# Performance work log

Hardware: AMD Instinct MI355X
Metric: run time of the kernel (lower is better)

Reference implementation:

```python
import jax, jax.numpy as jnp
import numpy as np
import math

POOL = 7          # RoIAlign output_size
SR = 2            # sampling_ratio


def _roi_align(feat, boxes, bidx):
    """torchvision RoIAlign, aligned=False, spatial_scale=1.0, sampling_ratio=2.
    feat: [B,C,H,W]; boxes: [N,4] (x1,y1,x2,y2) in pixel coords of this level;
    bidx: [N] int batch indices. Returns [N,C,POOL,POOL]."""
    B, C, H, W = feat.shape
    x1, y1, x2, y2 = boxes[:, 0], boxes[:, 1], boxes[:, 2], boxes[:, 3]
    roi_w = jnp.maximum(x2 - x1, 1.0)
    roi_h = jnp.maximum(y2 - y1, 1.0)
    bin_w = roi_w / POOL
    bin_h = roi_h / POOL
    # sample-point offsets within the ROI, in bin units: [POOL, SR]
    off = jnp.arange(POOL, dtype=feat.dtype)[:, None] + (jnp.arange(SR, dtype=feat.dtype)[None, :] + 0.5) / SR
    ys = y1[:, None, None] + bin_h[:, None, None] * off  # [N,POOL,SR]
    xs = x1[:, None, None] + bin_w[:, None, None] * off  # [N,POOL,SR]

    def prep(c, size):
        valid = (c > -1.0) & (c < size)
        c = jnp.clip(c, 0.0, size - 1)
        lo = jnp.floor(c).astype(jnp.int32)
        hi = jnp.minimum(lo + 1, size - 1)
        return lo, hi, c - lo, valid

    y_lo, y_hi, fy, vy = prep(ys, H)
    x_lo, x_hi, fx, vx = prep(xs, W)

    b = bidx.astype(jnp.int32)[:, None, None, None, None]  # [N,1,1,1,1]

    def gather(yi, xi):
        # -> [N,POOL,SR,POOL,SR,C] (advanced indices broadcast, channel slice last)
        return feat[b, :, yi[:, :, :, None, None], xi[:, None, None, :, :]]

    hy = (1.0 - fy)[:, :, :, None, None, None]
    ly = fy[:, :, :, None, None, None]
    hx = (1.0 - fx)[:, None, None, :, :, None]
    lx = fx[:, None, None, :, :, None]
    v = (gather(y_lo, x_lo) * hy * hx + gather(y_lo, x_hi) * hy * lx
         + gather(y_hi, x_lo) * ly * hx + gather(y_hi, x_hi) * ly * lx)
    valid = (vy[:, :, :, None, None] & vx[:, None, None, :, :])[..., None]
    v = jnp.where(valid, v, 0.0)
    out = v.mean(axis=(2, 4))          # average over SRxSR samples -> [N,POOL,POOL,C]
    return out.transpose(0, 3, 1, 2)   # [N,C,POOL,POOL]


def setup_inputs() -> dict:
    key = jax.random.key(0)
    k2, k3, k4, k5, kxy, kwh, kbi = jax.random.split(key, 7)
    N = 1000
    p2 = jax.random.normal(k2, (2, 256, 256, 256), dtype=jnp.float32)
    p3 = jax.random.normal(k3, (2, 256, 128, 128), dtype=jnp.float32)
    p4 = jax.random.normal(k4, (2, 256, 64, 64), dtype=jnp.float32)
    p5 = jax.random.normal(k5, (2, 256, 32, 32), dtype=jnp.float32)
    xy = jax.random.uniform(kxy, (N, 2), minval=0.0, maxval=0.7)
    wh = jax.random.uniform(kwh, (N, 2), minval=0.02, maxval=0.3)
    rpn_bbox = jnp.concatenate([xy, xy + wh], axis=1)  # (x1,y1,x2,y2) normalized
    box_index = jax.random.randint(kbi, (N,), 0, 2, dtype=jnp.int32)
    return {"p2": p2, "p3": p3, "p4": p4, "p5": p5,
            "rpn_bbox": rpn_bbox, "box_index": box_index}


def reference(p2, p3, p4, p5, rpn_bbox, box_index):
    feats = [p2, p3, p4, p5]
    N = rpn_bbox.shape[0]
    x1, y1, x2, y2 = rpn_bbox[:, 0], rpn_bbox[:, 1], rpn_bbox[:, 2], rpn_bbox[:, 3]
    area = (y2 - y1) * (x2 - x1)
    roi_level = jnp.log(jnp.sqrt(area)) / math.log(2.0)
    roi_level = jnp.clip(jnp.round(roi_level) + 4.0, 0.0, 3.0).astype(jnp.int32)
    # Compute RoIAlign of every ROI at every level, then select per-ROI level.
    # (The masked-select / per-level dispatch / argsort-combine in the original
    # restores original ROI order, so this is mathematically identical.)
    pooled_per_level = jnp.stack(
        [_roi_align(f, rpn_bbox * f.shape[3], box_index) for f in feats], axis=0
    )  # [4, N, C, 7, 7]
    pooled = pooled_per_level[roi_level, jnp.arange(N)]  # [N, C, 7, 7]
    return pooled
```

## Files before the change

### kernel.cpp

```cpp
#include <hip/hip_runtime.h>
#include <math.h>

#define POOL 7
#define NCELL 49
#define NCH 256
#define CH_SPLIT 8
#define CHPB (NCH / CH_SPLIT)
#define CHPW (CHPB / 4)
#define LDSF 640
#define NIT_S 10

typedef __attribute__((address_space(1))) void global_void;
typedef __attribute__((address_space(3))) void lds_void;
__device__ __forceinline__ void stage4(const float* g, float* l) {
    __builtin_amdgcn_global_load_lds((global_void*)g, (lds_void*)l, 4, 0, 0);
}
__device__ __forceinline__ void stage16(const float* g, float* l) {
    __builtin_amdgcn_global_load_lds((global_void*)g, (lds_void*)l, 16, 0, 0);
}

struct Tab {
    int loff0[4], loff1[4];
    float w00[4], w01[4], w10[4], w11[4];
};

__device__ __forceinline__ void make_tab(Tab& tb, int lane, int W, int rs, int xb, int y0,
                                         float x1, float y1, float bin_w, float bin_h)
{
    int cell = (lane < NCELL) ? lane : (NCELL - 1);
    int py = cell / POOL, px = cell % POOL;
#pragma unroll
    for (int s = 0; s < 4; ++s) {
        int sy = s >> 1, sx = s & 1;
        float y = y1 + bin_h * ((float)py + ((float)sy + 0.5f) * 0.5f);
        float x = x1 + bin_w * ((float)px + ((float)sx + 0.5f) * 0.5f);
        bool v = (y > -1.f) && (y < (float)W) && (x > -1.f) && (x < (float)W);
        float yc = fminf(fmaxf(y, 0.f), (float)(W - 1));
        float xc = fminf(fmaxf(x, 0.f), (float)(W - 1));
        int ylo = (int)floorf(yc), xlo = (int)floorf(xc);
        int yhi = min(ylo + 1, W - 1);
        float fy = yc - (float)ylo, fx = xc - (float)xlo;
        float vv = v ? 0.25f : 0.f;
        int bxp = min(xlo, W - 2);
        bool in = (xlo == bxp);
        float wx0 = in ? (1.f - fx) : 0.f;
        float wx1 = in ? fx : 1.f;
        float wr0 = (1.f - fy) * vv, wr1 = fy * vv;
        tb.loff0[s] = (ylo - y0) * rs + (bxp - xb);
        tb.loff1[s] = (yhi - y0) * rs + (bxp - xb);
        tb.w00[s] = wr0 * wx0; tb.w01[s] = wr0 * wx1;
        tb.w10[s] = wr1 * wx0; tb.w11[s] = wr1 * wx1;
    }
}

__device__ __forceinline__ float consume(const float* cb, const Tab& tb)
{
    float acc = 0.f;
#pragma unroll
    for (int s = 0; s < 4; ++s) {
        float a0 = cb[tb.loff0[s]], a1 = cb[tb.loff0[s] + 1];
        float b0 = cb[tb.loff1[s]], b1 = cb[tb.loff1[s] + 1];
        acc += tb.w00[s] * a0 + tb.w01[s] * a1 + tb.w10[s] * b0 + tb.w11[s] * b1;
    }
    return acc;
}

template <int NIT4>
__device__ __forceinline__ void box_x4(
    const float* fbase, float* outp, float* sm, int lane,
    int W, int HW, int wwa, int y0, int x0a, int ngrp,
    float x1, float y1, float bin_w, float bin_h)
{
    int g_off[NIT4];
    bool act[NIT4];
    int wwa4 = wwa >> 2;
#pragma unroll
    for (int k = 0; k < NIT4; ++k) {
        int idx = k * 64 + lane;
        act[k] = idx < ngrp;
        int ii = act[k] ? idx : 0;
        int r = ii / wwa4;
        int c = ii - r * wwa4;
        g_off[k] = (y0 + r) * W + x0a + c * 4;
    }
#pragma unroll
    for (int k = 0; k < NIT4; ++k)
        if (act[k]) stage16(fbase + g_off[k], sm + k * 256);

    Tab tb;
    make_tab(tb, lane, W, wwa, x0a, y0, x1, y1, bin_w, bin_h);

#pragma unroll 2
    for (int i = 0; i < CHPW; ++i) {
        if (i + 1 < CHPW) {
            const float* fc = fbase + (size_t)(i + 1) * HW;
            float* nb = sm + ((i + 1) & 1) * LDSF;
#pragma unroll
            for (int k = 0; k < NIT4; ++k)
                if (act[k]) stage16(fc + g_off[k], nb + k * 256);
            if constexpr (NIT4 == 1) asm volatile("s_waitcnt vmcnt(1)" ::: "memory");
            else if constexpr (NIT4 == 2) asm volatile("s_waitcnt vmcnt(2)" ::: "memory");
            else                          asm volatile("s_waitcnt vmcnt(3)" ::: "memory");
        } else {
            asm volatile("s_waitcnt vmcnt(0)" ::: "memory");
        }
        float acc = consume(sm + (i & 1) * LDSF, tb);
        if (lane < NCELL)
            __builtin_nontemporal_store(acc, outp + (size_t)i * NCELL);
    }
}

__device__ __forceinline__ void box_s(
    const float* fbase, float* outp, float* sm, int lane,
    int W, int HW, int ww, int y0, int x0, int packed,
    float x1, float y1, float bin_w, float bin_h)
{
    int g_off[NIT_S];
#pragma unroll
    for (int k = 0; k < NIT_S; ++k) {
        int idx = k * 64 + lane;
        idx = (idx < packed) ? idx : 0;
        int r = idx / ww;
        int c = idx - r * ww;
        g_off[k] = (y0 + r) * W + (x0 + c);
    }
#pragma unroll
    for (int k = 0; k < NIT_S; ++k) stage4(fbase + g_off[k], sm + k * 64);

    Tab tb;
    make_tab(tb, lane, W, ww, x0, y0, x1, y1, bin_w, bin_h);

#pragma unroll 2
    for (int i = 0; i < CHPW; ++i) {
        if (i + 1 < CHPW) {
            const float* fc = fbase + (size_t)(i + 1) * HW;
            float* nb = sm + ((i + 1) & 1) * LDSF;
#pragma unroll
            for (int k = 0; k < NIT_S; ++k) stage4(fc + g_off[k], nb + k * 64);
            asm volatile("s_waitcnt vmcnt(10)" ::: "memory");
        } else {
            asm volatile("s_waitcnt vmcnt(0)" ::: "memory");
        }
        float acc = consume(sm + (i & 1) * LDSF, tb);
        if (lane < NCELL)
            __builtin_nontemporal_store(acc, outp + (size_t)i * NCELL);
    }
}

__global__ __launch_bounds__(256, 8) void roi_align_fpn_kernel(
    const float* __restrict__ p2, const float* __restrict__ p3,
    const float* __restrict__ p4, const float* __restrict__ p5,
    const float* __restrict__ boxes, const int* __restrict__ bidx,
    float* __restrict__ out, int N)
{
    __shared__ float smem[4][2][LDSF];
    const int n = blockIdx.y;
    const int t = threadIdx.x;
    const int wave = t >> 6;
    const int lane = t & 63;

    float bx1 = boxes[4 * n + 0], by1 = boxes[4 * n + 1];
    float bx2 = boxes[4 * n + 2], by2 = boxes[4 * n + 3];
    float area = (by2 - by1) * (bx2 - bx1);
    float lvlf = logf(sqrtf(area)) * 1.4426950408889634f;
    int level = (int)fminf(fmaxf(rintf(lvlf) + 4.0f, 0.0f), 3.0f);
    int W = 256 >> level;
    int HW = W * W;
    float scale = (float)W;
    float x1 = bx1 * scale, y1 = by1 * scale;
    float bin_w = fmaxf((bx2 - bx1) * scale, 1.0f) * (1.0f / POOL);
    float bin_h = fmaxf((by2 - by1) * scale, 1.0f) * (1.0f / POOL);

    const float* feat = (level == 0) ? p2 : (level == 1) ? p3 : (level == 2) ? p4 : p5;
    feat += (size_t)bidx[n] * NCH * HW;

    float yA = y1 + bin_h * 0.25f, yB = y1 + bin_h * 6.75f;
    float xA = x1 + bin_w * 0.25f, xB = x1 + bin_w * 6.75f;
    int y0  = (int)floorf(fminf(fmaxf(yA, 0.f), (float)(W - 1)));
    int y1h = min((int)floorf(fminf(fmaxf(yB, 0.f), (float)(W - 1))) + 1, W - 1);
    int x0  = (int)floorf(fminf(fmaxf(xA, 0.f), (float)(W - 1)));
    x0 = min(x0, W - 2);
    int x1p = min((int)floorf(fminf(fmaxf(xB, 0.f), (float)(W - 1))) + 1, W - 1);
    int ww = x1p - x0 + 1;
    int wh = y1h - y0 + 1;

    int x0a = x0 & ~3;
    int wwa = ((x1p - x0a + 1) + 3) & ~3;
    if ((wwa & 15) == 0) wwa += 4;
    int padded = wwa * wh;

    const int ch0 = blockIdx.x * CHPB + wave * CHPW;
    const float* fbase = feat + (size_t)ch0 * HW;
    float* sm = &smem[wave][0][0];
    int cell = (lane < NCELL) ? lane : (NCELL - 1);
    float* outp = out + (size_t)n * NCH * NCELL + (size_t)ch0 * NCELL + cell;

    if (padded <= LDSF) {
        int ngrp = (wwa >> 2) * wh;
        int nit4 = (ngrp + 63) >> 6;
        if (nit4 == 1)      box_x4<1>(fbase, outp, sm, lane, W, HW, wwa, y0, x0a, ngrp, x1, y1, bin_w, bin_h);
        else if (nit4 == 2) box_x4<2>(fbase, outp, sm, lane, W, HW, wwa, y0, x0a, ngrp, x1, y1, bin_w, bin_h);
        else                box_x4<3>(fbase, outp, sm, lane, W, HW, wwa, y0, x0a, ngrp, x1, y1, bin_w, bin_h);
    } else {
        int whc = min(wh, LDSF / ww);
        int packed = ww * whc;
        box_s(fbase, outp, sm, lane, W, HW, ww, y0, x0, packed, x1, y1, bin_w, bin_h);
    }
}

extern "C" void kernel_launch(void* const* d_in, const int* in_sizes, int n_in,
                              void* d_out, int out_size, void* d_ws, size_t ws_size,
                              hipStream_t stream) {
    const float* p2    = (const float*)d_in[0];
    const float* p3    = (const float*)d_in[1];
    const float* p4    = (const float*)d_in[2];
    const float* p5    = (const float*)d_in[3];
    const float* boxes = (const float*)d_in[4];
    const int*   bidx  = (const int*)d_in[5];
    float* out = (float*)d_out;
    int N = in_sizes[5];
    dim3 grid(CH_SPLIT, N);
    roi_align_fpn_kernel<<<grid, 256, 0, stream>>>(p2, p3, p4, p5, boxes, bidx, out, N);
}
```

Measured before the change: 274.5 us.

## Sort ROIs by level, batch and spatial bucket for cache locality; peel first iteration

Adds a single-block counting-sort kernel that orders boxes by FPN level, batch index and a coarse 8x8 center grid, then indexes the main kernel through this permutation. Spatially nearby ROIs run close together in time so their overlapping feature windows are more likely to hit in L2/MALL. The first channel iteration of both staging loops is also peeled, and the vmcnt waits are changed to allow one more outstanding operation, leaving the previous iteration's store in flight. The cost is an extra serial one-block launch and an indirection load per block.

```diff
diff --git a/kernel.cpp b/kernel.cpp
--- a/kernel.cpp
+++ b/kernel.cpp
@@ -9,6 +9,7 @@
 #define CHPW (CHPB / 4)
 #define LDSF 640
 #define NIT_S 10
+#define NBUCK 512
 
 typedef __attribute__((address_space(1))) void global_void;
 typedef __attribute__((address_space(3))) void lds_void;
@@ -17,6 +18,16 @@
 }
 __device__ __forceinline__ void stage16(const float* g, float* l) {
     __builtin_amdgcn_global_load_lds((global_void*)g, (lds_void*)l, 16, 0, 0);
+}
+
+template <int V> __device__ __forceinline__ void vwait() {
+    if constexpr (V == 0)  asm volatile("s_waitcnt vmcnt(0)" ::: "memory");
+    else if constexpr (V == 1)  asm volatile("s_waitcnt vmcnt(1)" ::: "memory");
+    else if constexpr (V == 2)  asm volatile("s_waitcnt vmcnt(2)" ::: "memory");
+    else if constexpr (V == 3)  asm volatile("s_waitcnt vmcnt(3)" ::: "memory");
+    else if constexpr (V == 4)  asm volatile("s_waitcnt vmcnt(4)" ::: "memory");
+    else if constexpr (V == 10) asm volatile("s_waitcnt vmcnt(10)" ::: "memory");
+    else if constexpr (V == 11) asm volatile("s_waitcnt vmcnt(11)" ::: "memory");
 }
 
 struct Tab {
@@ -90,19 +101,27 @@
     Tab tb;
     make_tab(tb, lane, W, wwa, x0a, y0, x1, y1, bin_w, bin_h);
 
+    {
+        const float* fc = fbase + (size_t)HW;
+        float* nb = sm + LDSF;
+#pragma unroll
+        for (int k = 0; k < NIT4; ++k)
+            if (act[k]) stage16(fc + g_off[k], nb + k * 256);
+        vwait<NIT4>();
+        float acc = consume(sm, tb);
+        if (lane < NCELL) __builtin_nontemporal_store(acc, outp);
+    }
 #pragma unroll 2
-    for (int i = 0; i < CHPW; ++i) {
+    for (int i = 1; i < CHPW; ++i) {
         if (i + 1 < CHPW) {
             const float* fc = fbase + (size_t)(i + 1) * HW;
             float* nb = sm + ((i + 1) & 1) * LDSF;
 #pragma unroll
             for (int k = 0; k < NIT4; ++k)
                 if (act[k]) stage16(fc + g_off[k], nb + k * 256);
-            if constexpr (NIT4 == 1) asm volatile("s_waitcnt vmcnt(1)" ::: "memory");
-            else if constexpr (NIT4 == 2) asm volatile("s_waitcnt vmcnt(2)" ::: "memory");
-            else                          asm volatile("s_waitcnt vmcnt(3)" ::: "memory");
+            vwait<NIT4 + 1>();
         } else {
-            asm volatile("s_waitcnt vmcnt(0)" ::: "memory");
+            vwait<1>();
         }
         float acc = consume(sm + (i & 1) * LDSF, tb);
         if (lane < NCELL)
@@ -130,16 +149,25 @@
     Tab tb;
     make_tab(tb, lane, W, ww, x0, y0, x1, y1, bin_w, bin_h);
 
+    {
+        const float* fc = fbase + (size_t)HW;
+        float* nb = sm + LDSF;
+#pragma unroll
+        for (int k = 0; k < NIT_S; ++k) stage4(fc + g_off[k], nb + k * 64);
+        vwait<NIT_S>();
+        float acc = consume(sm, tb);
+        if (lane < NCELL) __builtin_nontemporal_store(acc, outp);
+    }
 #pragma unroll 2
-    for (int i = 0; i < CHPW; ++i) {
+    for (int i = 1; i < CHPW; ++i) {
         if (i + 1 < CHPW) {
             const float* fc = fbase + (size_t)(i + 1) * HW;
             float* nb = sm + ((i + 1) & 1) * LDSF;
 #pragma unroll
             for (int k = 0; k < NIT_S; ++k) stage4(fc + g_off[k], nb + k * 64);
-            asm volatile("s_waitcnt vmcnt(10)" ::: "memory");
+            vwait<NIT_S + 1>();
         } else {
-            asm volatile("s_waitcnt vmcnt(0)" ::: "memory");
+            vwait<1>();
         }
         float acc = consume(sm + (i & 1) * LDSF, tb);
         if (lane < NCELL)
@@ -147,14 +175,54 @@
     }
 }
 
+__device__ __forceinline__ int box_key(const float* boxes, const int* bidx, int n)
+{
+    float bx1 = boxes[4 * n + 0], by1 = boxes[4 * n + 1];
+    float bx2 = boxes[4 * n + 2], by2 = boxes[4 * n + 3];
+    float area = (by2 - by1) * (bx2 - bx1);
+    float lvlf = logf(sqrtf(area)) * 1.4426950408889634f;
+    int level = (int)fminf(fmaxf(rintf(lvlf) + 4.0f, 0.0f), 3.0f);
+    int b = bidx[n] & 1;
+    float cx = 0.5f * (bx1 + bx2), cy = 0.5f * (by1 + by2);
+    int qx = min(7, max(0, (int)(cx * 8.0f)));
+    int qy = min(7, max(0, (int)(cy * 8.0f)));
+    return (((((level << 1) | b) << 3) | qy) << 3) | qx;
+}
+
+__global__ __launch_bounds__(NBUCK) void box_sort_kernel(
+    const float* __restrict__ boxes, const int* __restrict__ bidx,
+    int* __restrict__ perm, int N)
+{
+    __shared__ int h0[NBUCK], h1[NBUCK];
+    const int t = threadIdx.x;
+    h0[t] = 0;
+    __syncthreads();
+    for (int n = t; n < N; n += NBUCK)
+        atomicAdd(&h0[box_key(boxes, bidx, n)], 1);
+    __syncthreads();
+    int* src = h0; int* dst = h1;
+    for (int off = 1; off < NBUCK; off <<= 1) {
+        dst[t] = src[t] + ((t >= off) ? src[t - off] : 0);
+        __syncthreads();
+        int* tmp = src; src = dst; dst = tmp;
+    }
+    dst[t] = (t == 0) ? 0 : src[t - 1];
+    __syncthreads();
+    for (int n = t; n < N; n += NBUCK) {
+        int slot = atomicAdd(&dst[box_key(boxes, bidx, n)], 1);
+        perm[slot] = n;
+    }
+}
+
 __global__ __launch_bounds__(256, 8) void roi_align_fpn_kernel(
     const float* __restrict__ p2, const float* __restrict__ p3,
     const float* __restrict__ p4, const float* __restrict__ p5,
     const float* __restrict__ boxes, const int* __restrict__ bidx,
+    const int* __restrict__ perm,
     float* __restrict__ out, int N)
 {
     __shared__ float smem[4][2][LDSF];
-    const int n = blockIdx.y;
+    const int n = perm ? perm[blockIdx.y] : (int)blockIdx.y;
     const int t = threadIdx.x;
     const int wave = t >> 6;
     const int lane = t & 63;
@@ -219,6 +287,11 @@
     const int*   bidx  = (const int*)d_in[5];
     float* out = (float*)d_out;
     int N = in_sizes[5];
+    int* perm = nullptr;
+    if (d_ws && ws_size >= (size_t)N * sizeof(int)) {
+        perm = (int*)d_ws;
+        box_sort_kernel<<<1, NBUCK, 0, stream>>>(boxes, bidx, perm, N);
+    }
     dim3 grid(CH_SPLIT, N);
-    roi_align_fpn_kernel<<<grid, 256, 0, stream>>>(p2, p3, p4, p5, boxes, bidx, out, N);
-}
+    roi_align_fpn_kernel<<<grid, 256, 0, stream>>>(p2, p3, p4, p5, boxes, bidx, perm, out, N);
+}
```

New measurement: 293.6 us. 1.07x slower.
